# Optimization experiments

Hardware: AMD Instinct MI355X
Metric: run time of the kernel (lower is better)

## Reference

```python
import jax, jax.numpy as jnp
import numpy as np

B, L, H, I, K, G = 2, 4096, 1024, 2048, 4, 8  # batch, seq, hidden, intermediate, kernel, conv groups
EPS = 1e-5


def setup_inputs() -> dict:
    key = jax.random.key(0)
    ks = jax.random.split(key, 8)
    s = 0.02
    return {
        "hidden_states": jax.random.normal(ks[0], (B, L, H), jnp.float32),
        "in_proj_w": jax.random.normal(ks[1], (2 * I, H), jnp.float32) * s,  # Linear(H -> 2I), no bias
        "conv_w": jax.random.normal(ks[2], (I, I // G, K), jnp.float32) * s,  # grouped Conv1d weight [O, I/G, K]
        "conv_b": jax.random.normal(ks[3], (I,), jnp.float32) * s,
        "ln_g": jnp.ones((I,), jnp.float32),
        "ln_b": jnp.zeros((I,), jnp.float32),
        "fc_w": jax.random.normal(ks[4], (H, I), jnp.float32) * s,   # MLP c_fc: I -> H
        "fc_b": jnp.zeros((H,), jnp.float32),
        "cproj_w": jax.random.normal(ks[5], (I, H), jnp.float32) * s,  # MLP c_proj: H -> I
        "cproj_b": jnp.zeros((I,), jnp.float32),
        "out_w": jax.random.normal(ks[6], (H, I), jnp.float32) * s,  # out_proj: I -> H, no bias
    }


def _layernorm(x, g, b):
    m = x.mean(-1, keepdims=True)
    v = jnp.var(x, axis=-1, keepdims=True)
    return (x - m) * jax.lax.rsqrt(v + EPS) * g + b


def reference(hidden_states, in_proj_w, conv_w, conv_b, ln_g, ln_b, fc_w, fc_b, cproj_w, cproj_b, out_w):
    # in_proj then chunk into hidden / gate (torch chunks along channel dim after transpose)
    p = hidden_states @ in_proj_w.T              # [B, L, 2I]
    h, gate = p[..., :I], p[..., I:]             # [B, L, I] each
    gate = jax.nn.silu(gate)
    # causal grouped conv1d: ConstantPad1d((K-1, 0)) + Conv1d(groups=G)
    hc = jnp.transpose(h, (0, 2, 1))             # [B, I, L]
    conv = jax.lax.conv_general_dilated(
        hc, conv_w, window_strides=(1,), padding=[(K - 1, 0)],
        feature_group_count=G, dimension_numbers=("NCH", "OIH", "NCH"))
    conv = conv + conv_b[None, :, None]          # [B, I, L]
    h = jnp.transpose(conv, (0, 2, 1)) * gate    # gated mixing, [B, L, I]
    residual = h
    hn = _layernorm(h, ln_g, ln_b)
    # MLP (dropout is identity at inference): I -> H -> silu -> I
    m = jax.nn.silu(hn @ fc_w.T + fc_b) @ cproj_w.T + cproj_b
    h = m + residual
    return h @ out_w.T                           # [B, L, H]
```

## Files before the change

kernel.cpp:

```cpp
#include <hip/hip_runtime.h>
#include <stdint.h>


#define TOKENS 8192
#define HDIM   1024
#define IDIM   2048
#define PADL   4099

typedef __bf16 bf16_t;
typedef __bf16 bf16x8 __attribute__((ext_vector_type(8)));
typedef __bf16 bf16x4 __attribute__((ext_vector_type(4)));
typedef float  f32x4  __attribute__((ext_vector_type(4)));

__device__ __forceinline__ float silu_f(float v) { return v / (1.f + __expf(-v)); }

__global__ __launch_bounds__(256) void cvt_f32_bf16(const float* __restrict__ in,
                                                    bf16_t* __restrict__ out, int n4) {
  int i = blockIdx.x * 256 + threadIdx.x;
  if (i < n4) {
    float4 v = reinterpret_cast<const float4*>(in)[i];
    bf16x4 o = {(bf16_t)v.x, (bf16_t)v.y, (bf16_t)v.z, (bf16_t)v.w};
    reinterpret_cast<bf16x4*>(out)[i] = o;
  }
}

__global__ __launch_bounds__(256) void expand_convw(const float* __restrict__ cw,
                                                    bf16_t* __restrict__ w2) {
  int idx = blockIdx.x * 256 + threadIdx.x;
  int o = idx >> 10;
  int r = idx & 1023;
  int k = r >> 8;
  int ci = r & 255;
  w2[idx] = (bf16_t)cw[(o << 10) + (ci << 2) + k];
}

__global__ __launch_bounds__(256) void zero_pad_rows(bf16_t* __restrict__ hpad) {
  int idx = blockIdx.x * 256 + threadIdx.x;
  if (idx < 2 * 3 * IDIM) {
    int b = idx / (3 * IDIM);
    int r = idx - b * (3 * IDIM);
    hpad[(size_t)b * PADL * IDIM + r] = (bf16_t)0.f;
  }
}

__global__ __launch_bounds__(256) void ln_k(const bf16_t* __restrict__ x,
                                            const float* __restrict__ g,
                                            const float* __restrict__ b,
                                            bf16_t* __restrict__ out) {
  int row = blockIdx.x;
  int tid = threadIdx.x;
  const bf16_t* xr = x + (size_t)row * IDIM;
  bf16x8 v = *reinterpret_cast<const bf16x8*>(xr + tid * 8);
  float f[8];
  float s = 0.f, ss = 0.f;
#pragma unroll
  for (int j = 0; j < 8; ++j) { f[j] = (float)v[j]; s += f[j]; ss += f[j] * f[j]; }
#pragma unroll
  for (int o = 32; o; o >>= 1) { s += __shfl_xor(s, o); ss += __shfl_xor(ss, o); }
  __shared__ float red[2][4];
  int wv = tid >> 6, lane = tid & 63;
  if (lane == 0) { red[0][wv] = s; red[1][wv] = ss; }
  __syncthreads();
  s  = red[0][0] + red[0][1] + red[0][2] + red[0][3];
  ss = red[1][0] + red[1][1] + red[1][2] + red[1][3];
  float mean = s * (1.f / IDIM);
  float var  = ss * (1.f / IDIM) - mean * mean;
  float rstd = rsqrtf(var + 1e-5f);
  bf16x8 o8;
#pragma unroll
  for (int j = 0; j < 8; ++j) {
    int c = tid * 8 + j;
    o8[j] = (bf16_t)((f[j] - mean) * rstd * g[c] + b[c]);
  }
  *reinterpret_cast<bf16x8*>(out + (size_t)row * IDIM + tid * 8) = o8;
}

template <int KIND, int N, int K>
__global__ __launch_bounds__(256, 2) void gemm_k(
    const bf16_t* __restrict__ A, const bf16_t* __restrict__ W,
    const float* __restrict__ bias, const bf16_t* __restrict__ extra,
    void* __restrict__ outp, bf16_t* __restrict__ hpad_out,
    bf16_t* __restrict__ gate_out) {
  __shared__ bf16_t As[128][64];
  __shared__ bf16_t Bs[128][64];
  const int tid  = threadIdx.x;
  const int lane = tid & 63;
  const int wv   = tid >> 6;
  const int wr   = wv >> 1, wc = wv & 1;
  constexpr int nTilesN = N / 128;
  const int t0 = (blockIdx.x / nTilesN) * 128;
  const int n0 = (blockIdx.x % nTilesN) * 128;

  f32x4 acc[4][4] = {};

  for (int kt = 0; kt < K / 64; ++kt) {
    const int k0 = kt * 64;
#pragma unroll
    for (int i = 0; i < 4; ++i) {
      int lin = i * 256 + tid;
      int r = lin >> 3, c = (lin & 7) << 3;
      const bf16_t* src;
      if constexpr (KIND == 1) {
        int row = t0 + r;
        int b = row >> 12, pos = row & 4095;
        int tap = k0 >> 8, cc = k0 & 255;
        int g = n0 >> 8;
        src = A + ((size_t)b * PADL + pos + tap) * IDIM + g * 256 + cc + c;
      } else {
        src = A + (size_t)(t0 + r) * K + k0 + c;
      }
      __builtin_amdgcn_global_load_lds(
          (const __attribute__((address_space(1))) void*)src,
          (__attribute__((address_space(3))) void*)&As[r][c], 16, 0, 0);
    }
#pragma unroll
    for (int i = 0; i < 4; ++i) {
      int lin = i * 256 + tid;
      int r = lin >> 3, c = (lin & 7) << 3;
      const bf16_t* src = W + (size_t)(n0 + r) * K + k0 + c;
      __builtin_amdgcn_global_load_lds(
          (const __attribute__((address_space(1))) void*)src,
          (__attribute__((address_space(3))) void*)&Bs[r][c], 16, 0, 0);
    }
    __syncthreads();
#pragma unroll
    for (int s = 0; s < 2; ++s) {
      bf16x8 af[4], bfv[4];
#pragma unroll
      for (int mi = 0; mi < 4; ++mi)
        af[mi] = *reinterpret_cast<const bf16x8*>(
            &As[wr * 64 + mi * 16 + (lane & 15)][s * 32 + (lane >> 4) * 8]);
#pragma unroll
      for (int ni = 0; ni < 4; ++ni)
        bfv[ni] = *reinterpret_cast<const bf16x8*>(
            &Bs[wc * 64 + ni * 16 + (lane & 15)][s * 32 + (lane >> 4) * 8]);
#pragma unroll
      for (int mi = 0; mi < 4; ++mi)
#pragma unroll
        for (int ni = 0; ni < 4; ++ni)
          acc[mi][ni] = __builtin_amdgcn_mfma_f32_16x16x32_bf16(
              af[mi], bfv[ni], acc[mi][ni], 0, 0, 0);
    }
    __syncthreads();
  }

#pragma unroll
  for (int mi = 0; mi < 4; ++mi) {
#pragma unroll
    for (int ni = 0; ni < 4; ++ni) {
      const int col = n0 + wc * 64 + ni * 16 + (lane & 15);
      float bv = 0.f;
      if constexpr (KIND == 1 || KIND == 2 || KIND == 3) bv = bias[col];
#pragma unroll
      for (int r = 0; r < 4; ++r) {
        const int row = t0 + wr * 64 + mi * 16 + (lane >> 4) * 4 + r;
        float v = acc[mi][ni][r];
        if constexpr (KIND == 0) {
          if (n0 < IDIM) {
            int b = row >> 12, pos = row & 4095;
            hpad_out[((size_t)b * PADL + 3 + pos) * IDIM + col] = (bf16_t)v;
          } else {
            gate_out[(size_t)row * IDIM + (col - IDIM)] = (bf16_t)silu_f(v);
          }
        } else if constexpr (KIND == 1) {
          float gt = (float)extra[(size_t)row * IDIM + col];
          ((bf16_t*)outp)[(size_t)row * N + col] = (bf16_t)((v + bv) * gt);
        } else if constexpr (KIND == 2) {
          ((bf16_t*)outp)[(size_t)row * N + col] = (bf16_t)silu_f(v + bv);
        } else if constexpr (KIND == 3) {
          float res = (float)extra[(size_t)row * N + col];
          ((bf16_t*)outp)[(size_t)row * N + col] = (bf16_t)(v + bv + res);
        } else {
          ((float*)outp)[(size_t)row * N + col] = v;
        }
      }
    }
  }
}

extern "C" void kernel_launch(void* const* d_in, const int* in_sizes, int n_in,
                              void* d_out, int out_size, void* d_ws, size_t ws_size,
                              hipStream_t stream) {
  const float* hs       = (const float*)d_in[0];
  const float* in_projw = (const float*)d_in[1];
  const float* conv_w   = (const float*)d_in[2];
  const float* conv_b   = (const float*)d_in[3];
  const float* ln_g     = (const float*)d_in[4];
  const float* ln_b     = (const float*)d_in[5];
  const float* fc_w     = (const float*)d_in[6];
  const float* fc_b     = (const float*)d_in[7];
  const float* cproj_w  = (const float*)d_in[8];
  const float* cproj_b  = (const float*)d_in[9];
  const float* out_w    = (const float*)d_in[10];

  char* ws = (char*)d_ws;
  size_t off = 0;
  auto alloc = [&](size_t bytes) {
    char* p = ws + off;
    off += (bytes + 255) & ~(size_t)255;
    return p;
  };
  bf16_t* hs_b  = (bf16_t*)alloc((size_t)TOKENS * HDIM * 2);
  bf16_t* w_ip  = (bf16_t*)alloc((size_t)2 * IDIM * HDIM * 2);
  bf16_t* w2c   = (bf16_t*)alloc((size_t)IDIM * 1024 * 2);
  bf16_t* w_fc  = (bf16_t*)alloc((size_t)HDIM * IDIM * 2);
  bf16_t* w_cp  = (bf16_t*)alloc((size_t)IDIM * HDIM * 2);
  bf16_t* w_out = (bf16_t*)alloc((size_t)HDIM * IDIM * 2);
  bf16_t* hpad  = (bf16_t*)alloc((size_t)2 * PADL * IDIM * 2);
  bf16_t* gate  = (bf16_t*)alloc((size_t)TOKENS * IDIM * 2);
  bf16_t* xres  = (bf16_t*)alloc((size_t)TOKENS * IDIM * 2);

  bf16_t* t_buf = hs_b;
  bf16_t* hn    = gate;
  bf16_t* h2    = hpad;

  cvt_f32_bf16<<<8192, 256, 0, stream>>>(hs, hs_b, TOKENS * HDIM / 4);
  cvt_f32_bf16<<<4096, 256, 0, stream>>>(in_projw, w_ip, 2 * IDIM * HDIM / 4);
  cvt_f32_bf16<<<2048, 256, 0, stream>>>(fc_w, w_fc, HDIM * IDIM / 4);
  cvt_f32_bf16<<<2048, 256, 0, stream>>>(cproj_w, w_cp, IDIM * HDIM / 4);
  cvt_f32_bf16<<<2048, 256, 0, stream>>>(out_w, w_out, HDIM * IDIM / 4);
  expand_convw<<<8192, 256, 0, stream>>>(conv_w, w2c);
  zero_pad_rows<<<48, 256, 0, stream>>>(hpad);

  gemm_k<0, 4096, 1024><<<64 * 32, 256, 0, stream>>>(hs_b, w_ip, nullptr, nullptr,
                                                     nullptr, hpad, gate);
  gemm_k<1, 2048, 1024><<<64 * 16, 256, 0, stream>>>(hpad, w2c, conv_b, gate,
                                                     xres, nullptr, nullptr);
  ln_k<<<TOKENS, 256, 0, stream>>>(xres, ln_g, ln_b, hn);
  gemm_k<2, 1024, 2048><<<64 * 8, 256, 0, stream>>>(hn, w_fc, fc_b, nullptr,
                                                    t_buf, nullptr, nullptr);
  gemm_k<3, 2048, 1024><<<64 * 16, 256, 0, stream>>>(t_buf, w_cp, cproj_b, xres,
                                                     h2, nullptr, nullptr);
  gemm_k<4, 1024, 2048><<<64 * 8, 256, 0, stream>>>(h2, w_out, nullptr, nullptr,
                                                    d_out, nullptr, nullptr);
}
```

Baseline: 460.7 us.

## Rewrite GEMM with double-buffered LDS, swizzle, interleaved staging, larger tiles, fused weight cast

The GEMM kernel now double-buffers its LDS tiles and interleaves global-to-LDS loads for the next K step with four quadrant MFMA phases. These phases are separated by barriers, with raised wave priority during the math. It adds an XOR swizzle on LDS rows to cut bank conflicts, remaps block IDs across 8 XCD-style partitions, and uses 256x256 tiles with 8 waves for the larger GEMMs. The four weight-conversion launches are merged into one kernel. The gains come from overlapping memory with compute and getting more reuse per tile, at the cost of more LDS use, which limits occupancy, and more complex waitcnt logic.

```diff
diff --git a/kernel.cpp b/kernel.cpp
--- a/kernel.cpp
+++ b/kernel.cpp
@@ -24,13 +24,26 @@
   }
 }
 
+__global__ __launch_bounds__(256) void cvt_weights(
+    const float* __restrict__ ipf, const float* __restrict__ fcf,
+    const float* __restrict__ cpf, const float* __restrict__ outf,
+    bf16_t* __restrict__ ipb, bf16_t* __restrict__ fcb,
+    bf16_t* __restrict__ cpb, bf16_t* __restrict__ outb) {
+  int i = blockIdx.x * 256 + threadIdx.x;
+  const float* src; bf16_t* dst; int off;
+  if (i < 1048576)      { src = ipf;  dst = ipb;  off = i; }
+  else if (i < 1572864) { src = fcf;  dst = fcb;  off = i - 1048576; }
+  else if (i < 2097152) { src = cpf;  dst = cpb;  off = i - 1572864; }
+  else                  { src = outf; dst = outb; off = i - 2097152; }
+  float4 v = reinterpret_cast<const float4*>(src)[off];
+  bf16x4 o = {(bf16_t)v.x, (bf16_t)v.y, (bf16_t)v.z, (bf16_t)v.w};
+  reinterpret_cast<bf16x4*>(dst)[off] = o;
+}
+
 __global__ __launch_bounds__(256) void expand_convw(const float* __restrict__ cw,
                                                     bf16_t* __restrict__ w2) {
   int idx = blockIdx.x * 256 + threadIdx.x;
-  int o = idx >> 10;
-  int r = idx & 1023;
-  int k = r >> 8;
-  int ci = r & 255;
+  int o = idx >> 10, r = idx & 1023, k = r >> 8, ci = r & 255;
   w2[idx] = (bf16_t)cw[(o << 10) + (ci << 2) + k];
 }
 
@@ -47,12 +60,10 @@
                                             const float* __restrict__ g,
                                             const float* __restrict__ b,
                                             bf16_t* __restrict__ out) {
-  int row = blockIdx.x;
-  int tid = threadIdx.x;
+  int row = blockIdx.x, tid = threadIdx.x;
   const bf16_t* xr = x + (size_t)row * IDIM;
   bf16x8 v = *reinterpret_cast<const bf16x8*>(xr + tid * 8);
-  float f[8];
-  float s = 0.f, ss = 0.f;
+  float f[8], s = 0.f, ss = 0.f;
 #pragma unroll
   for (int j = 0; j < 8; ++j) { f[j] = (float)v[j]; s += f[j]; ss += f[j] * f[j]; }
 #pragma unroll
@@ -75,85 +86,148 @@
   *reinterpret_cast<bf16x8*>(out + (size_t)row * IDIM + tid * 8) = o8;
 }
 
-template <int KIND, int N, int K>
-__global__ __launch_bounds__(256, 2) void gemm_k(
+#define BARR __builtin_amdgcn_s_barrier()
+
+template <int KIND, int N, int K, int BM, int BN, int WM, int WN>
+__global__ __launch_bounds__(WM * WN * 64, 2) void gemm_k(
     const bf16_t* __restrict__ A, const bf16_t* __restrict__ W,
     const float* __restrict__ bias, const bf16_t* __restrict__ extra,
     void* __restrict__ outp, bf16_t* __restrict__ hpad_out,
     bf16_t* __restrict__ gate_out) {
-  __shared__ bf16_t As[128][64];
-  __shared__ bf16_t Bs[128][64];
-  const int tid  = threadIdx.x;
-  const int lane = tid & 63;
-  const int wv   = tid >> 6;
-  const int wr   = wv >> 1, wc = wv & 1;
-  constexpr int nTilesN = N / 128;
-  const int t0 = (blockIdx.x / nTilesN) * 128;
-  const int n0 = (blockIdx.x % nTilesN) * 128;
-
-  f32x4 acc[4][4] = {};
-
-  for (int kt = 0; kt < K / 64; ++kt) {
-    const int k0 = kt * 64;
-#pragma unroll
-    for (int i = 0; i < 4; ++i) {
-      int lin = i * 256 + tid;
-      int r = lin >> 3, c = (lin & 7) << 3;
-      const bf16_t* src;
-      if constexpr (KIND == 1) {
-        int row = t0 + r;
-        int b = row >> 12, pos = row & 4095;
-        int tap = k0 >> 8, cc = k0 & 255;
-        int g = n0 >> 8;
-        src = A + ((size_t)b * PADL + pos + tap) * IDIM + g * 256 + cc + c;
-      } else {
-        src = A + (size_t)(t0 + r) * K + k0 + c;
-      }
-      __builtin_amdgcn_global_load_lds(
-          (const __attribute__((address_space(1))) void*)src,
-          (__attribute__((address_space(3))) void*)&As[r][c], 16, 0, 0);
+  constexpr int TM = BM / WM, TN = BN / WN;
+  constexpr int MR = TM / 16, NR = TN / 16;
+  constexpr int NT = K / 64;
+  constexpr int NTN = N / BN;
+  __shared__ bf16_t As[2][BM][64];
+  __shared__ bf16_t Bs[2][BN][64];
+  const int tid = threadIdx.x, lane = tid & 63, wid = tid >> 6;
+  const int wr = wid / WN, wc = wid % WN;
+  int bid = blockIdx.x;
+  { const int cpx = gridDim.x >> 3; bid = (bid & 7) * cpx + (bid >> 3); }
+  const int t0 = (bid / NTN) * BM, n0 = (bid % NTN) * BN;
+
+  const int sw16 = (((lane & 7) ^ (lane >> 3)) << 4);
+
+  int cur = 0;
+
+  auto stageA = [&](int j, int tt) {
+    const int row = wr * TM + j * (TM / 4) + (wc << 3) + (lane >> 3);
+    char* dst = (char*)&As[tt & 1][0][0] + row * 128 + ((lane & 7) << 4);
+    const char* src;
+    if constexpr (KIND == 1) {
+      const int grow = t0 + row, b = grow >> 12, pos = grow & 4095;
+      src = (const char*)A +
+            (((size_t)b * PADL + pos + (tt >> 2)) * IDIM + (n0 & ~255) + ((tt & 3) << 6)) * 2 + sw16;
+    } else {
+      src = (const char*)A + ((size_t)(t0 + row) * K + tt * 64) * 2 + sw16;
     }
-#pragma unroll
-    for (int i = 0; i < 4; ++i) {
-      int lin = i * 256 + tid;
-      int r = lin >> 3, c = (lin & 7) << 3;
-      const bf16_t* src = W + (size_t)(n0 + r) * K + k0 + c;
-      __builtin_amdgcn_global_load_lds(
-          (const __attribute__((address_space(1))) void*)src,
-          (__attribute__((address_space(3))) void*)&Bs[r][c], 16, 0, 0);
+    __builtin_amdgcn_global_load_lds((const __attribute__((address_space(1))) void*)src,
+                                     (__attribute__((address_space(3))) void*)dst, 16, 0, 0);
+  };
+  auto stageB = [&](int j, int tt) {
+    const int row = wc * TN + j * (TN / 4) + (wr << 3) + (lane >> 3);
+    char* dst = (char*)&Bs[tt & 1][0][0] + row * 128 + ((lane & 7) << 4);
+    const char* src = (const char*)W + ((size_t)(n0 + row) * K + tt * 64) * 2 + sw16;
+    __builtin_amdgcn_global_load_lds((const __attribute__((address_space(1))) void*)src,
+                                     (__attribute__((address_space(3))) void*)dst, 16, 0, 0);
+  };
+  auto readA = [&](int mi, int s) -> bf16x8 {
+    const int row = wr * TM + mi * 16 + (lane & 15);
+    const int cb = (s * 64 + ((lane >> 4) << 4)) ^ ((lane & 7) << 4);
+    return *(const bf16x8*)((const char*)&As[cur][0][0] + row * 128 + cb);
+  };
+  auto readB = [&](int ni, int s) -> bf16x8 {
+    const int row = wc * TN + ni * 16 + (lane & 15);
+    const int cb = (s * 64 + ((lane >> 4) << 4)) ^ ((lane & 7) << 4);
+    return *(const bf16x8*)((const char*)&Bs[cur][0][0] + row * 128 + cb);
+  };
+
+  f32x4 acc[MR][NR] = {};
+  bf16x8 aF[MR / 2][2], bF[NR][2];
+
+#define MMA_QUAD(MH, NH)                                                        \
+  _Pragma("unroll") for (int mi = 0; mi < MR / 2; ++mi) {                       \
+    _Pragma("unroll") for (int ni = 0; ni < NR / 2; ++ni) {                     \
+      _Pragma("unroll") for (int s = 0; s < 2; ++s) {                           \
+        acc[(MH) * (MR / 2) + mi][(NH) * (NR / 2) + ni] =                       \
+            __builtin_amdgcn_mfma_f32_16x16x32_bf16(                            \
+                aF[mi][s], bF[(NH) * (NR / 2) + ni][s],                         \
+                acc[(MH) * (MR / 2) + mi][(NH) * (NR / 2) + ni], 0, 0, 0);      \
+      }                                                                         \
+    }                                                                           \
+  }
+
+#pragma unroll
+  for (int j = 0; j < 4; ++j) stageA(j, 0);
+#pragma unroll
+  for (int j = 0; j < 4; ++j) stageB(j, 0);
+  asm volatile("s_waitcnt vmcnt(2)");
+  BARR;
+
+  for (int t = 0; t < NT; ++t) {
+    cur = t & 1;
+    const bool nx = (t + 1) < NT;
+#pragma unroll
+    for (int mi = 0; mi < MR / 2; ++mi)
+#pragma unroll
+      for (int s = 0; s < 2; ++s) aF[mi][s] = readA(mi, s);
+#pragma unroll
+    for (int ni = 0; ni < NR / 2; ++ni)
+#pragma unroll
+      for (int s = 0; s < 2; ++s) bF[ni][s] = readB(ni, s);
+    if (nx) {
+      stageA(0, t + 1); stageA(1, t + 1);
+      asm volatile("s_waitcnt vmcnt(2)");
+    } else {
+      asm volatile("s_waitcnt vmcnt(0)");
     }
-    __syncthreads();
-#pragma unroll
-    for (int s = 0; s < 2; ++s) {
-      bf16x8 af[4], bfv[4];
-#pragma unroll
-      for (int mi = 0; mi < 4; ++mi)
-        af[mi] = *reinterpret_cast<const bf16x8*>(
-            &As[wr * 64 + mi * 16 + (lane & 15)][s * 32 + (lane >> 4) * 8]);
-#pragma unroll
-      for (int ni = 0; ni < 4; ++ni)
-        bfv[ni] = *reinterpret_cast<const bf16x8*>(
-            &Bs[wc * 64 + ni * 16 + (lane & 15)][s * 32 + (lane >> 4) * 8]);
-#pragma unroll
-      for (int mi = 0; mi < 4; ++mi)
-#pragma unroll
-        for (int ni = 0; ni < 4; ++ni)
-          acc[mi][ni] = __builtin_amdgcn_mfma_f32_16x16x32_bf16(
-              af[mi], bfv[ni], acc[mi][ni], 0, 0, 0);
+    BARR;
+    __builtin_amdgcn_s_setprio(1);
+    MMA_QUAD(0, 0);
+    __builtin_amdgcn_s_setprio(0);
+    BARR;
+#pragma unroll
+    for (int ni = 0; ni < NR / 2; ++ni)
+#pragma unroll
+      for (int s = 0; s < 2; ++s) bF[NR / 2 + ni][s] = readB(NR / 2 + ni, s);
+    if (nx) { stageA(2, t + 1); stageA(3, t + 1); }
+    BARR;
+    __builtin_amdgcn_s_setprio(1);
+    MMA_QUAD(0, 1);
+    __builtin_amdgcn_s_setprio(0);
+    BARR;
+#pragma unroll
+    for (int mi = 0; mi < MR / 2; ++mi)
+#pragma unroll
+      for (int s = 0; s < 2; ++s) aF[mi][s] = readA(MR / 2 + mi, s);
+    if (nx) { stageB(0, t + 1); stageB(1, t + 1); }
+    BARR;
+    __builtin_amdgcn_s_setprio(1);
+    MMA_QUAD(1, 1);
+    __builtin_amdgcn_s_setprio(0);
+    BARR;
+    if (nx) {
+      stageB(2, t + 1); stageB(3, t + 1);
+      asm volatile("s_waitcnt vmcnt(2)");
     }
-    __syncthreads();
-  }
-
-#pragma unroll
-  for (int mi = 0; mi < 4; ++mi) {
-#pragma unroll
-    for (int ni = 0; ni < 4; ++ni) {
-      const int col = n0 + wc * 64 + ni * 16 + (lane & 15);
+    BARR;
+    __builtin_amdgcn_s_setprio(1);
+    MMA_QUAD(1, 0);
+    __builtin_amdgcn_s_setprio(0);
+    BARR;
+  }
+#undef MMA_QUAD
+
+#pragma unroll
+  for (int mi = 0; mi < MR; ++mi) {
+#pragma unroll
+    for (int ni = 0; ni < NR; ++ni) {
+      const int col = n0 + wc * TN + ni * 16 + (lane & 15);
       float bv = 0.f;
       if constexpr (KIND == 1 || KIND == 2 || KIND == 3) bv = bias[col];
 #pragma unroll
       for (int r = 0; r < 4; ++r) {
-        const int row = t0 + wr * 64 + mi * 16 + (lane >> 4) * 4 + r;
+        const int row = t0 + wr * TM + mi * 16 + ((lane >> 4) << 2) + r;
         float v = acc[mi][ni][r];
         if constexpr (KIND == 0) {
           if (n0 < IDIM) {
@@ -215,22 +289,20 @@
   bf16_t* h2    = hpad;
 
   cvt_f32_bf16<<<8192, 256, 0, stream>>>(hs, hs_b, TOKENS * HDIM / 4);
-  cvt_f32_bf16<<<4096, 256, 0, stream>>>(in_projw, w_ip, 2 * IDIM * HDIM / 4);
-  cvt_f32_bf16<<<2048, 256, 0, stream>>>(fc_w, w_fc, HDIM * IDIM / 4);
-  cvt_f32_bf16<<<2048, 256, 0, stream>>>(cproj_w, w_cp, IDIM * HDIM / 4);
-  cvt_f32_bf16<<<2048, 256, 0, stream>>>(out_w, w_out, HDIM * IDIM / 4);
+  cvt_weights<<<10240, 256, 0, stream>>>(in_projw, fc_w, cproj_w, out_w,
+                                         w_ip, w_fc, w_cp, w_out);
   expand_convw<<<8192, 256, 0, stream>>>(conv_w, w2c);
   zero_pad_rows<<<48, 256, 0, stream>>>(hpad);
 
-  gemm_k<0, 4096, 1024><<<64 * 32, 256, 0, stream>>>(hs_b, w_ip, nullptr, nullptr,
-                                                     nullptr, hpad, gate);
-  gemm_k<1, 2048, 1024><<<64 * 16, 256, 0, stream>>>(hpad, w2c, conv_b, gate,
-                                                     xres, nullptr, nullptr);
+  gemm_k<0, 4096, 1024, 256, 256, 2, 4><<<512, 512, 0, stream>>>(
+      hs_b, w_ip, nullptr, nullptr, nullptr, hpad, gate);
+  gemm_k<1, 2048, 1024, 256, 256, 2, 4><<<256, 512, 0, stream>>>(
+      hpad, w2c, conv_b, gate, xres, nullptr, nullptr);
   ln_k<<<TOKENS, 256, 0, stream>>>(xres, ln_g, ln_b, hn);
-  gemm_k<2, 1024, 2048><<<64 * 8, 256, 0, stream>>>(hn, w_fc, fc_b, nullptr,
-                                                    t_buf, nullptr, nullptr);
-  gemm_k<3, 2048, 1024><<<64 * 16, 256, 0, stream>>>(t_buf, w_cp, cproj_b, xres,
-                                                     h2, nullptr, nullptr);
-  gemm_k<4, 1024, 2048><<<64 * 8, 256, 0, stream>>>(h2, w_out, nullptr, nullptr,
-                                                    d_out, nullptr, nullptr);
-}
+  gemm_k<2, 1024, 2048, 128, 128, 2, 2><<<512, 256, 0, stream>>>(
+      hn, w_fc, fc_b, nullptr, t_buf, nullptr, nullptr);
+  gemm_k<3, 2048, 1024, 256, 256, 2, 4><<<256, 512, 0, stream>>>(
+      t_buf, w_cp, cproj_b, xres, h2, nullptr, nullptr);
+  gemm_k<4, 1024, 2048, 128, 128, 2, 2><<<512, 256, 0, stream>>>(
+      h2, w_out, nullptr, nullptr, d_out, nullptr, nullptr);
+}
```

New measurement: 414.9 us. 1.11x faster.
